# Kernel optimization log

Measured on AMD Instinct MI355X. Metric: run time of the kernel, lower is better.

The kernel has to match this reference:

```python
import jax, jax.numpy as jnp
import numpy as np

D = 512  # token_dim == hidden_dim
K = 65536  # number of trajectory tokens


def safe_normalize(v, eps=1e-6):
    n = jnp.linalg.norm(v, axis=-1, keepdims=True)
    ok = n > eps
    e1 = jnp.zeros_like(v).at[..., 0].set(1.0)
    return jnp.where(ok, v / jnp.maximum(n, eps), e1)


def rot6d_to_matrix(x, eps=1e-6):
    # x: (K, 6) -> R: (K, 3, 3), rows (a1, b2, a3)
    a1 = safe_normalize(x[..., 0:3], eps)
    a2 = x[..., 3:6]
    proj = jnp.sum(a1 * a2, axis=-1, keepdims=True) * a1
    b2 = safe_normalize(a2 - proj, eps)
    a3 = safe_normalize(jnp.cross(a1, b2), eps)
    b2 = safe_normalize(jnp.cross(a3, a1), eps)
    return jnp.stack((a1, b2, a3), axis=-2)


def geodesic_angle(R_pred, R_gt, eps=1e-8):
    # RtR = R_gt^T @ R_pred, per-element (K,3,3)
    RtR = jnp.einsum('kji,kjl->kil', R_gt, R_pred)
    trace = RtR[..., 0, 0] + RtR[..., 1, 1] + RtR[..., 2, 2]
    c = jnp.clip((trace - 1.0) * 0.5, -1.0 + 1e-6, 1.0 - 1e-6)
    skew = RtR - jnp.swapaxes(RtR, -1, -2)
    v = jnp.stack([skew[..., 2, 1], skew[..., 0, 2], skew[..., 1, 0]], axis=-1)
    s = 0.5 * jnp.linalg.norm(v, axis=-1) + eps
    return jnp.arctan2(s, c)


def huber(pred, target, beta, mask):
    # smooth-L1 with beta, masked mean (denominator = clamped mask sum)
    d = jnp.abs(pred - target)
    l = jnp.where(d < beta, 0.5 * d * d / beta, d - 0.5 * beta) * mask
    return l.sum() / jnp.maximum(mask.sum(), 1.0)


def rot_loss_fn(pred, gt):
    # pred, gt: (K, 12) = [L rot6d(6), R rot6d(6)]
    Lp, Rp = pred[:, :6], pred[:, 6:]
    Lt, Rt = gt[:, :6], gt[:, 6:]
    Lvalid = jnp.all(Lt != -1000.0, axis=-1)
    Rvalid = jnp.all(Rt != -1000.0, axis=-1)
    safe6 = jnp.array([1.0, 0.0, 0.0, 0.0, 1.0, 0.0], pred.dtype)
    Lt = jnp.where(Lvalid[:, None], Lt, safe6)
    Rt = jnp.where(Rvalid[:, None], Rt, safe6)
    ang_L = geodesic_angle(rot6d_to_matrix(Lp), rot6d_to_matrix(Lt))
    ang_R = geodesic_angle(rot6d_to_matrix(Rp), rot6d_to_matrix(Rt))
    wL = Lvalid.astype(pred.dtype)
    wR = Rvalid.astype(pred.dtype)
    denom = jnp.maximum(wL.sum() + wR.sum(), 1e-8)
    num = jnp.sum(wL * jnp.where(Lvalid, ang_L, 0.0)) + jnp.sum(wR * jnp.where(Rvalid, ang_R, 0.0))
    return num / denom


def _heads(hidden_states, w1, b1, w2, b2, w3, b3):
    # 4 stacked MLPs (m = time, coord, coord2d, quat), torch Linear layout (out, in)
    h1 = jax.nn.relu(jnp.einsum('kc,mhc->mkh', hidden_states, w1) + b1[:, None, :])
    h2 = jax.nn.relu(jnp.einsum('mkh,mgh->mkg', h1, w2) + b2[:, None, :])
    pred_time = h2[0] @ w3[0:1].T + b3[0:1]      # (K, 1)
    pred_coords = h2[1] @ w3[1:7].T + b3[1:7]    # (K, 6)
    pred_2d = h2[2] @ w3[7:11].T + b3[7:11]      # (K, 4)
    pred_quat = h2[3] @ w3[11:23].T + b3[11:23]  # (K, 12)
    return pred_time, pred_coords, pred_2d, pred_quat


def _loss(pred_time, pred_coords, pred_2d, pred_quat, gt,
          beta_3d=0.07, beta_2d=0.02, beta_time=3.0, sigma_time=3.0):
    time_gt = gt[:, 0:1]
    time_valid = (time_gt != -1000.0).astype(jnp.float32)
    xyz_gt = gt[:, 1:7]
    xyz_valid = (xyz_gt != -1000.0).astype(jnp.float32)
    uv_gt = gt[:, 7:11]
    uv_valid = (uv_gt != -1000.0).astype(jnp.float32)
    quat_gt = gt[:, 11:23]
    quat_valid = (quat_gt != -1000.0).astype(jnp.float32)

    time_loss = huber(pred_time, time_gt, beta_time, time_valid)

    dt = jnp.abs(pred_time - time_gt)
    w_t = jnp.where(time_valid.sum() > 0,
                    jnp.exp(-0.5 * (dt / sigma_time) ** 2) * time_valid,
                    jnp.ones_like(pred_time))  # (K, 1), broadcasts over feature dims

    loss_3d = huber(pred_coords, xyz_gt, beta_3d, xyz_valid * w_t)
    loss_2d = huber(pred_2d / 1408.0, uv_gt / 1408.0, beta_2d, uv_valid * w_t)
    quat_huber = huber(pred_quat, quat_gt, 0.2, quat_valid * w_t)
    rot_l = 0.15 * rot_loss_fn(pred_quat, quat_gt)

    return 1.0 * time_loss + 2.0 * loss_3d + 0.5 * loss_2d + 0.5 * quat_huber + rot_l


def setup_inputs() -> dict:
    key = jax.random.key(0)
    ks = jax.random.split(key, 6)
    s = 1.0 / np.sqrt(D)
    return {
        'hidden_states': jax.random.normal(ks[0], (K, D), jnp.float32),
        'gt_traj': jax.random.uniform(ks[1], (K, 23), jnp.float32),
        'w1': jax.random.normal(ks[2], (4, D, D), jnp.float32) * s,
        'b1': jnp.zeros((4, D), jnp.float32),
        'w2': jax.random.normal(ks[3], (4, D, D), jnp.float32) * s,
        'b2': jnp.zeros((4, D), jnp.float32),
        'w3': jax.random.normal(ks[4], (23, D), jnp.float32) * s,
        'b3': jnp.zeros((23,), jnp.float32),
    }


def reference(hidden_states, gt_traj, w1, b1, w2, b2, w3, b3):
    pred_time, pred_coords, pred_2d, pred_quat = _heads(hidden_states, w1, b1, w2, b2, w3, b3)
    total_loss = _loss(pred_time, pred_coords, pred_2d, pred_quat, gt_traj)
    packed = jnp.concatenate(
        [pred_coords.reshape(-1, 2, 3), pred_quat.reshape(-1, 2, 6)], axis=-1
    ).reshape(-1, 18)
    return pred_time, packed, total_loss
```

## Files before the change

kernel.cpp:

```cpp
#include <hip/hip_runtime.h>
#include <math.h>


#define KROWS 65536
#define DH 512

typedef _Float16 f16;
typedef _Float16 half8 __attribute__((ext_vector_type(8)));
typedef float floatx4 __attribute__((ext_vector_type(4)));

#define WS_WF16   0
#define WS_W3F16  4194304
#define WS_PRED2D 4227072
#define WS_PART   5275648

__global__ __launch_bounds__(256) void convert_weights(
    const float* __restrict__ w1, const float* __restrict__ w2,
    const float* __restrict__ w3, f16* __restrict__ wf16, f16* __restrict__ w3f16)
{
  int t = blockIdx.x * 256 + threadIdx.x;
  if (t < 262144) {
    int ml = t >> 15;
    int mm = ml >> 1, l = ml & 1;
    int r = t & 32767;
    int fb = r >> 6;
    int lane = r & 63;
    int nt = fb >> 4, kq = fb & 15;
    int n = nt * 16 + (lane & 15);
    int k = kq * 32 + (lane >> 4) * 8;
    const float* src = (l ? w2 : w1) + (size_t)mm * 262144 + n * 512 + k;
    floatx4 u0 = *(const floatx4*)(src);
    floatx4 u1 = *(const floatx4*)(src + 4);
    half8 h;
    h[0] = (f16)u0[0]; h[1] = (f16)u0[1]; h[2] = (f16)u0[2]; h[3] = (f16)u0[3];
    h[4] = (f16)u1[0]; h[5] = (f16)u1[1]; h[6] = (f16)u1[2]; h[7] = (f16)u1[3];
    *(half8*)(wf16 + (size_t)ml * 262144 + fb * 512 + lane * 8) = h;
  } else {
    int j = t - 262144;
    if (j < 23 * DH) w3f16[j] = (f16)w3[j];
  }
}

__global__ __launch_bounds__(512, 4)
__attribute__((amdgpu_waves_per_eu(4, 4)))
void fused_kernel(
    const float* __restrict__ hidden,
    const f16* __restrict__ wf16,
    const f16* __restrict__ w3f16,
    const float* __restrict__ b1g,
    const float* __restrict__ b2g,
    const float* __restrict__ b3g,
    float* __restrict__ dout,
    float* __restrict__ pred2d)
{
  __shared__ __align__(16) unsigned char smem[65536];

  const int bid = blockIdx.x;
  const int rr  = bid & 7;
  const int m   = rr >> 1;
  const int row_tile = ((bid >> 3) << 1) | (rr & 1);
  const int r0  = row_tile * 64;
  const int tid = threadIdx.x;
  const int w   = __builtin_amdgcn_readfirstlane(tid >> 6);
  const int lane = tid & 63;
  const int l15 = lane & 15;
  const int lg  = lane >> 4;

  const int arow = l15 * 128;
  const int ao   = (lg * 16) ^ ((l15 & 7) << 4);
  auto aread = [&](int g, int mt) -> half8 {
    return *(const half8*)(smem + (g >> 1) * 8192 + mt * 2048 + arow
                           + (ao ^ ((g & 1) << 6)));
  };
  const f16* bptr = wf16 + (size_t)(m * 2) * 262144 + lane * 8;
  auto bload = [&](int l, int g, int nt) -> half8 {
    return *(const half8*)(bptr + l * 262144 + ((w * 4 + nt) * 16 + g) * 512);
  };

  {
    const int row = tid >> 3;
    const int cg  = tid & 7;
    const int sw  = ((cg * 16) ^ ((row & 7) << 4));
    const float* hr = hidden + (size_t)(r0 + row) * DH + cg * 8;
    unsigned char* dst = smem + row * 128 + sw;
#pragma unroll
    for (int kc = 0; kc < 8; ++kc) {
      floatx4 u0 = *(const floatx4*)(hr + kc * 64);
      floatx4 u1 = *(const floatx4*)(hr + kc * 64 + 4);
      half8 p;
      p[0] = (f16)u0[0]; p[1] = (f16)u0[1]; p[2] = (f16)u0[2]; p[3] = (f16)u0[3];
      p[4] = (f16)u1[0]; p[5] = (f16)u1[1]; p[6] = (f16)u1[2]; p[7] = (f16)u1[3];
      *(half8*)(dst + kc * 8192) = p;
    }
  }

  floatx4 acc[4][4];
  const floatx4 zf = {0.f, 0.f, 0.f, 0.f};
  const half8 hz = {(f16)0, (f16)0, (f16)0, (f16)0, (f16)0, (f16)0, (f16)0, (f16)0};

  __syncthreads();

#pragma unroll
  for (int mt = 0; mt < 4; ++mt)
#pragma unroll
    for (int nt = 0; nt < 4; ++nt) acc[mt][nt] = zf;

  {
    half8 c0 = bload(0, 0, 0), c1 = bload(0, 0, 1),
          c2 = bload(0, 0, 2), c3 = bload(0, 0, 3);
#pragma unroll 1
    for (int g = 0; g < 16; ++g) {
      half8 n0, n1, n2, n3;
      if (g < 15) {
        n0 = bload(0, g + 1, 0); n1 = bload(0, g + 1, 1);
        n2 = bload(0, g + 1, 2); n3 = bload(0, g + 1, 3);
      }
#pragma unroll
      for (int mt = 0; mt < 4; ++mt) {
        half8 a = aread(g, mt);
        acc[mt][0] = __builtin_amdgcn_mfma_f32_16x16x32_f16(a, c0, acc[mt][0], 0, 0, 0);
        acc[mt][1] = __builtin_amdgcn_mfma_f32_16x16x32_f16(a, c1, acc[mt][1], 0, 0, 0);
        acc[mt][2] = __builtin_amdgcn_mfma_f32_16x16x32_f16(a, c2, acc[mt][2], 0, 0, 0);
        acc[mt][3] = __builtin_amdgcn_mfma_f32_16x16x32_f16(a, c3, acc[mt][3], 0, 0, 0);
      }
      c0 = n0; c1 = n1; c2 = n2; c3 = n3;
    }
  }

  __syncthreads();

  {
    unsigned char* myc = smem + w * 8192;
#pragma unroll
    for (int nt = 0; nt < 4; ++nt) {
      const float bv = b1g[m * DH + w * 64 + nt * 16 + l15];
      const int cb = 2 * (nt * 16 + l15);
#pragma unroll
      for (int mt = 0; mt < 4; ++mt)
#pragma unroll
        for (int j = 0; j < 4; ++j) {
          float v = fmaxf(acc[mt][nt][j] + bv, 0.f);
          int row = mt * 16 + 4 * lg + j;
          *(f16*)(myc + row * 128 + (cb ^ ((row & 7) << 4))) = (f16)v;
        }
    }
  }
  __syncthreads();

#pragma unroll
  for (int mt = 0; mt < 4; ++mt)
#pragma unroll
    for (int nt = 0; nt < 4; ++nt) acc[mt][nt] = zf;

  {
    half8 c0 = bload(1, 0, 0), c1 = bload(1, 0, 1),
          c2 = bload(1, 0, 2), c3 = bload(1, 0, 3);
#pragma unroll 1
    for (int g = 0; g < 16; ++g) {
      half8 n0, n1, n2, n3;
      if (g < 15) {
        n0 = bload(1, g + 1, 0); n1 = bload(1, g + 1, 1);
        n2 = bload(1, g + 1, 2); n3 = bload(1, g + 1, 3);
      }
#pragma unroll
      for (int mt = 0; mt < 4; ++mt) {
        half8 a = aread(g, mt);
        acc[mt][0] = __builtin_amdgcn_mfma_f32_16x16x32_f16(a, c0, acc[mt][0], 0, 0, 0);
        acc[mt][1] = __builtin_amdgcn_mfma_f32_16x16x32_f16(a, c1, acc[mt][1], 0, 0, 0);
        acc[mt][2] = __builtin_amdgcn_mfma_f32_16x16x32_f16(a, c2, acc[mt][2], 0, 0, 0);
        acc[mt][3] = __builtin_amdgcn_mfma_f32_16x16x32_f16(a, c3, acc[mt][3], 0, 0, 0);
      }
      c0 = n0; c1 = n1; c2 = n2; c3 = n3;
    }
  }

  __syncthreads();

  {
    unsigned char* myc = smem + w * 8192;
#pragma unroll
    for (int nt = 0; nt < 4; ++nt) {
      const float bv = b2g[m * DH + w * 64 + nt * 16 + l15];
      const int cb = 2 * (nt * 16 + l15);
#pragma unroll
      for (int mt = 0; mt < 4; ++mt)
#pragma unroll
        for (int j = 0; j < 4; ++j) {
          float v = fmaxf(acc[mt][nt][j] + bv, 0.f);
          int row = mt * 16 + 4 * lg + j;
          *(f16*)(myc + row * 128 + (cb ^ ((row & 7) << 4))) = (f16)v;
        }
    }
  }
  __syncthreads();

  if (w < 4) {
    const int base_m = (m == 0) ? 0 : (m == 1) ? 1 : (m == 2) ? 7 : 11;
    const int cnt_m  = (m == 0) ? 1 : (m == 1) ? 6 : (m == 2) ? 4 : 12;
    const bool ovalid = l15 < cnt_m;
    const f16* w3row = w3f16 + (size_t)(base_m + (ovalid ? l15 : 0)) * DH;
    floatx4 acc3 = zf;
#pragma unroll 2
    for (int q = 0; q < 16; ++q) {
      half8 ah = aread(q, w);
      half8 wv = ovalid ? *(const half8*)(w3row + q * 32 + lg * 8) : hz;
      acc3 = __builtin_amdgcn_mfma_f32_16x16x32_f16(ah, wv, acc3, 0, 0, 0);
    }
    if (ovalid) {
      const float bo = b3g[base_m + l15];
#pragma unroll
      for (int j = 0; j < 4; ++j) {
        const int row = r0 + w * 16 + 4 * lg + j;
        const float v = acc3[j] + bo;
        if (m == 0)      { if (l15 == 0) dout[row] = v; }
        else if (m == 1) { dout[KROWS + row * 18 + (l15 < 3 ? l15 : l15 + 6)] = v; }
        else if (m == 2) { pred2d[row * 4 + l15] = v; }
        else             { dout[KROWS + row * 18 + (l15 < 6 ? l15 + 3 : l15 + 6)] = v; }
      }
    }
  }
}

__device__ __forceinline__ void safe_norm3(float x, float y, float z, float* o) {
  float n = sqrtf(x * x + y * y + z * z);
  if (n > 1e-6f) { o[0] = x / n; o[1] = y / n; o[2] = z / n; }
  else           { o[0] = 1.f;   o[1] = 0.f;   o[2] = 0.f; }
}

__device__ __forceinline__ void rot6d(const float* x, float* R) {
  float a1[3]; safe_norm3(x[0], x[1], x[2], a1);
  float d = a1[0] * x[3] + a1[1] * x[4] + a1[2] * x[5];
  float b2[3]; safe_norm3(x[3] - d * a1[0], x[4] - d * a1[1], x[5] - d * a1[2], b2);
  float a3[3];
  safe_norm3(a1[1] * b2[2] - a1[2] * b2[1],
             a1[2] * b2[0] - a1[0] * b2[2],
             a1[0] * b2[1] - a1[1] * b2[0], a3);
  float bb[3];
  safe_norm3(a3[1] * a1[2] - a3[2] * a1[1],
             a3[2] * a1[0] - a3[0] * a1[2],
             a3[0] * a1[1] - a3[1] * a1[0], bb);
  R[0] = a1[0]; R[1] = a1[1]; R[2] = a1[2];
  R[3] = bb[0]; R[4] = bb[1]; R[5] = bb[2];
  R[6] = a3[0]; R[7] = a3[1]; R[8] = a3[2];
}

__device__ __forceinline__ float geo_angle(const float* P, const float* G) {
  float M[9];
#pragma unroll
  for (int i = 0; i < 3; ++i)
#pragma unroll
    for (int l = 0; l < 3; ++l)
      M[i * 3 + l] = G[0 + i] * P[0 + l] + G[3 + i] * P[3 + l] + G[6 + i] * P[6 + l];
  float tr = M[0] + M[4] + M[8];
  float c = fminf(fmaxf((tr - 1.f) * 0.5f, -1.f + 1e-6f), 1.f - 1e-6f);
  float v0 = M[7] - M[5], v1 = M[2] - M[6], v2 = M[3] - M[1];
  float s = 0.5f * sqrtf(v0 * v0 + v1 * v1 + v2 * v2) + 1e-8f;
  return atan2f(s, c);
}

__global__ __launch_bounds__(256) void loss_partial(
    const float* __restrict__ gt, const float* __restrict__ dout,
    const float* __restrict__ pred2d, float* __restrict__ partials)
{
  const int r = blockIdx.x * 256 + threadIdx.x;
  const float* g  = gt + (size_t)r * 23;
  const float* pk = dout + KROWS + (size_t)r * 18;
  float a[17];

  const float pt = dout[r];
  const float tg = g[0];
  const float tv = (tg != -1000.f) ? 1.f : 0.f;
  const float dt = fabsf(pt - tg);
  a[0] = ((dt < 3.f) ? (0.5f * dt * dt / 3.f) : (dt - 1.5f)) * tv;
  a[1] = tv;
  a[2] = tv;
  const float wt = expf(-0.5f * (dt / 3.f) * (dt / 3.f)) * tv;

  float n3T = 0.f, d3T = 0.f, n3F = 0.f, d3F = 0.f;
#pragma unroll
  for (int j = 0; j < 6; ++j) {
    const float p = pk[j < 3 ? j : j + 6];
    const float q = g[1 + j];
    const float val = (q != -1000.f) ? 1.f : 0.f;
    const float d = fabsf(p - q);
    const float l = (d < 0.07f) ? (0.5f * d * d / 0.07f) : (d - 0.035f);
    n3T += l * val * wt; d3T += val * wt; n3F += l * val; d3F += val;
  }
  a[3] = n3T; a[4] = d3T; a[5] = n3F; a[6] = d3F;

  float n2T = 0.f, d2T = 0.f, n2F = 0.f, d2F = 0.f;
#pragma unroll
  for (int j = 0; j < 4; ++j) {
    const float p = pred2d[(size_t)r * 4 + j];
    const float q = g[7 + j];
    const float val = (q != -1000.f) ? 1.f : 0.f;
    const float d = fabsf(p / 1408.f - q / 1408.f);
    const float l = (d < 0.02f) ? (0.5f * d * d / 0.02f) : (d - 0.01f);
    n2T += l * val * wt; d2T += val * wt; n2F += l * val; d2F += val;
  }
  a[7] = n2T; a[8] = d2T; a[9] = n2F; a[10] = d2F;

  float qp[12];
#pragma unroll
  for (int j = 0; j < 12; ++j) qp[j] = pk[j < 6 ? j + 3 : j + 6];
  float nqT = 0.f, dqT = 0.f, nqF = 0.f, dqF = 0.f;
#pragma unroll
  for (int j = 0; j < 12; ++j) {
    const float q = g[11 + j];
    const float val = (q != -1000.f) ? 1.f : 0.f;
    const float d = fabsf(qp[j] - q);
    const float l = (d < 0.2f) ? (0.5f * d * d / 0.2f) : (d - 0.1f);
    nqT += l * val * wt; dqT += val * wt; nqF += l * val; dqF += val;
  }
  a[11] = nqT; a[12] = dqT; a[13] = nqF; a[14] = dqF;

  bool Lv = true, Rv = true;
#pragma unroll
  for (int j = 0; j < 6; ++j) {
    if (g[11 + j] == -1000.f) Lv = false;
    if (g[17 + j] == -1000.f) Rv = false;
  }
  const float safe6[6] = {1.f, 0.f, 0.f, 0.f, 1.f, 0.f};
  float Lt[6], Rt[6];
#pragma unroll
  for (int j = 0; j < 6; ++j) {
    Lt[j] = Lv ? g[11 + j] : safe6[j];
    Rt[j] = Rv ? g[17 + j] : safe6[j];
  }
  float Rp[9], Rg[9];
  rot6d(qp, Rp);     rot6d(Lt, Rg);
  const float angL = geo_angle(Rp, Rg);
  rot6d(qp + 6, Rp); rot6d(Rt, Rg);
  const float angR = geo_angle(Rp, Rg);
  a[15] = (Lv ? angL : 0.f) + (Rv ? angR : 0.f);
  a[16] = (Lv ? 1.f : 0.f) + (Rv ? 1.f : 0.f);

#pragma unroll
  for (int i = 0; i < 17; ++i) {
    float v = a[i];
#pragma unroll
    for (int off = 32; off > 0; off >>= 1) v += __shfl_down(v, off, 64);
    a[i] = v;
  }
  __shared__ float red[4][17];
  if ((threadIdx.x & 63) == 0) {
    const int wv = threadIdx.x >> 6;
#pragma unroll
    for (int i = 0; i < 17; ++i) red[wv][i] = a[i];
  }
  __syncthreads();
  if (threadIdx.x < 17)
    partials[blockIdx.x * 20 + threadIdx.x] =
        red[0][threadIdx.x] + red[1][threadIdx.x] + red[2][threadIdx.x] + red[3][threadIdx.x];
}

__global__ void loss_final(const float* __restrict__ partials, float* __restrict__ dout)
{
  __shared__ float s[17];
  const int i = threadIdx.x;
  if (i < 17) {
    float v = 0.f;
    for (int b = 0; b < 256; ++b) v += partials[b * 20 + i];
    s[i] = v;
  }
  __syncthreads();
  if (i == 0) {
    const bool flag = s[2] > 0.f;
    const float time_loss = s[0] / fmaxf(s[1], 1.f);
    const float l3 = flag ? s[3] / fmaxf(s[4], 1.f) : s[5] / fmaxf(s[6], 1.f);
    const float l2 = flag ? s[7] / fmaxf(s[8], 1.f) : s[9] / fmaxf(s[10], 1.f);
    const float lq = flag ? s[11] / fmaxf(s[12], 1.f) : s[13] / fmaxf(s[14], 1.f);
    const float rot = 0.15f * (s[15] / fmaxf(s[16], 1e-8f));
    dout[19 * KROWS] = time_loss + 2.f * l3 + 0.5f * l2 + 0.5f * lq + rot;
  }
}

extern "C" void kernel_launch(void* const* d_in, const int* in_sizes, int n_in,
                              void* d_out, int out_size, void* d_ws, size_t ws_size,
                              hipStream_t stream) {
  (void)in_sizes; (void)n_in; (void)out_size; (void)ws_size;
  const float* hidden = (const float*)d_in[0];
  const float* gt     = (const float*)d_in[1];
  const float* w1     = (const float*)d_in[2];
  const float* b1     = (const float*)d_in[3];
  const float* w2     = (const float*)d_in[4];
  const float* b2     = (const float*)d_in[5];
  const float* w3     = (const float*)d_in[6];
  const float* b3     = (const float*)d_in[7];
  float* dout = (float*)d_out;

  unsigned char* ws = (unsigned char*)d_ws;
  f16*   wf16     = (f16*)(ws + WS_WF16);
  f16*   w3f16    = (f16*)(ws + WS_W3F16);
  float* pred2d   = (float*)(ws + WS_PRED2D);
  float* partials = (float*)(ws + WS_PART);

  convert_weights<<<1070, 256, 0, stream>>>(w1, w2, w3, wf16, w3f16);
  fused_kernel<<<4096, 512, 0, stream>>>(hidden, wf16, w3f16, b1, b2, b3, dout, pred2d);
  loss_partial<<<256, 256, 0, stream>>>(gt, dout, pred2d, partials);
  loss_final<<<1, 64, 0, stream>>>(partials, dout);
}
```

Baseline: 396.7 us.

## Switch hidden-layer GEMMs to 32x32x16 MFMA with matching weight layout

Replaces the 16x16x32 MFMA tiling of the two hidden-layer GEMMs with 32x32x16 MFMA instructions (2x2 tiles of 32x32 per wave). The pre-converted f16 weight layout and the LDS read pattern are changed to match the new operand fragments, and the epilogue row mapping is updated. The per-iteration B loads are no longer software-prefetched a step ahead but issued at the top of each of 8 K-steps. The intent is fewer MFMA issues and more operand reuse per instruction, at the risk of exposing global-load latency without the prefetch.

```diff
diff --git a/kernel.cpp b/kernel.cpp
--- a/kernel.cpp
+++ b/kernel.cpp
@@ -8,6 +8,7 @@
 typedef _Float16 f16;
 typedef _Float16 half8 __attribute__((ext_vector_type(8)));
 typedef float floatx4 __attribute__((ext_vector_type(4)));
+typedef float floatx16 __attribute__((ext_vector_type(16)));
 
 #define WS_WF16   0
 #define WS_W3F16  4194304
@@ -25,9 +26,9 @@
     int r = t & 32767;
     int fb = r >> 6;
     int lane = r & 63;
-    int nt = fb >> 4, kq = fb & 15;
-    int n = nt * 16 + (lane & 15);
-    int k = kq * 32 + (lane >> 4) * 8;
+    int nt = fb >> 5, ks = fb & 31;
+    int n = nt * 32 + (lane & 31);
+    int k = ks * 16 + (lane >> 5) * 8;
     const float* src = (l ? w2 : w1) + (size_t)mm * 262144 + n * 512 + k;
     floatx4 u0 = *(const floatx4*)(src);
     floatx4 u1 = *(const floatx4*)(src + 4);
@@ -65,16 +66,26 @@
   const int lane = tid & 63;
   const int l15 = lane & 15;
   const int lg  = lane >> 4;
-
-  const int arow = l15 * 128;
-  const int ao   = (lg * 16) ^ ((l15 & 7) << 4);
-  auto aread = [&](int g, int mt) -> half8 {
-    return *(const half8*)(smem + (g >> 1) * 8192 + mt * 2048 + arow
-                           + (ao ^ ((g & 1) << 6)));
+  const int l31 = lane & 31;
+  const int hi  = lane >> 5;
+
+  const int arow32 = l31 * 128;
+  const int hi16   = hi * 16;
+  const int sw31   = (lane & 7) << 4;
+  auto aread32 = [&](int g, int mt, int ks) -> half8 {
+    return *(const half8*)(smem + g * 8192 + mt * 4096 + arow32
+                           + ((ks * 32 + hi16) ^ sw31));
+  };
+  const int arow16 = l15 * 128;
+  const int ao16   = (lg * 16) ^ ((l15 & 7) << 4);
+  auto aread16 = [&](int q, int mt) -> half8 {
+    return *(const half8*)(smem + (q >> 1) * 8192 + mt * 2048 + arow16
+                           + (ao16 ^ ((q & 1) << 6)));
   };
   const f16* bptr = wf16 + (size_t)(m * 2) * 262144 + lane * 8;
-  auto bload = [&](int l, int g, int nt) -> half8 {
-    return *(const half8*)(bptr + l * 262144 + ((w * 4 + nt) * 16 + g) * 512);
+  auto bload = [&](int l, int g, int ks, int nt) -> half8 {
+    return *(const half8*)(bptr + l * 262144
+                           + (((2 * w + nt) * 32) + (g * 4 + ks)) * 512);
   };
 
   {
@@ -94,36 +105,33 @@
     }
   }
 
-  floatx4 acc[4][4];
-  const floatx4 zf = {0.f, 0.f, 0.f, 0.f};
+  floatx16 acc[2][2];
   const half8 hz = {(f16)0, (f16)0, (f16)0, (f16)0, (f16)0, (f16)0, (f16)0, (f16)0};
 
   __syncthreads();
 
 #pragma unroll
-  for (int mt = 0; mt < 4; ++mt)
-#pragma unroll
-    for (int nt = 0; nt < 4; ++nt) acc[mt][nt] = zf;
-
-  {
-    half8 c0 = bload(0, 0, 0), c1 = bload(0, 0, 1),
-          c2 = bload(0, 0, 2), c3 = bload(0, 0, 3);
+  for (int mt = 0; mt < 2; ++mt)
+#pragma unroll
+    for (int nt = 0; nt < 2; ++nt)
+#pragma unroll
+      for (int e = 0; e < 16; ++e) acc[mt][nt][e] = 0.f;
+
 #pragma unroll 1
-    for (int g = 0; g < 16; ++g) {
-      half8 n0, n1, n2, n3;
-      if (g < 15) {
-        n0 = bload(0, g + 1, 0); n1 = bload(0, g + 1, 1);
-        n2 = bload(0, g + 1, 2); n3 = bload(0, g + 1, 3);
+  for (int g = 0; g < 8; ++g) {
+    half8 b[2][4];
+#pragma unroll
+    for (int nt = 0; nt < 2; ++nt)
+#pragma unroll
+      for (int ks = 0; ks < 4; ++ks) b[nt][ks] = bload(0, g, ks, nt);
+#pragma unroll
+    for (int ks = 0; ks < 4; ++ks) {
+#pragma unroll
+      for (int mt = 0; mt < 2; ++mt) {
+        half8 a = aread32(g, mt, ks);
+        acc[mt][0] = __builtin_amdgcn_mfma_f32_32x32x16_f16(a, b[0][ks], acc[mt][0], 0, 0, 0);
+        acc[mt][1] = __builtin_amdgcn_mfma_f32_32x32x16_f16(a, b[1][ks], acc[mt][1], 0, 0, 0);
       }
-#pragma unroll
-      for (int mt = 0; mt < 4; ++mt) {
-        half8 a = aread(g, mt);
-        acc[mt][0] = __builtin_amdgcn_mfma_f32_16x16x32_f16(a, c0, acc[mt][0], 0, 0, 0);
-        acc[mt][1] = __builtin_amdgcn_mfma_f32_16x16x32_f16(a, c1, acc[mt][1], 0, 0, 0);
-        acc[mt][2] = __builtin_amdgcn_mfma_f32_16x16x32_f16(a, c2, acc[mt][2], 0, 0, 0);
-        acc[mt][3] = __builtin_amdgcn_mfma_f32_16x16x32_f16(a, c3, acc[mt][3], 0, 0, 0);
-      }
-      c0 = n0; c1 = n1; c2 = n2; c3 = n3;
     }
   }
 
@@ -132,15 +140,15 @@
   {
     unsigned char* myc = smem + w * 8192;
 #pragma unroll
-    for (int nt = 0; nt < 4; ++nt) {
-      const float bv = b1g[m * DH + w * 64 + nt * 16 + l15];
-      const int cb = 2 * (nt * 16 + l15);
-#pragma unroll
-      for (int mt = 0; mt < 4; ++mt)
-#pragma unroll
-        for (int j = 0; j < 4; ++j) {
-          float v = fmaxf(acc[mt][nt][j] + bv, 0.f);
-          int row = mt * 16 + 4 * lg + j;
+    for (int nt = 0; nt < 2; ++nt) {
+      const float bv = b1g[m * DH + w * 64 + nt * 32 + l31];
+      const int cb = 2 * (nt * 32 + l31);
+#pragma unroll
+      for (int mt = 0; mt < 2; ++mt)
+#pragma unroll
+        for (int e = 0; e < 16; ++e) {
+          float v = fmaxf(acc[mt][nt][e] + bv, 0.f);
+          int row = mt * 32 + (e & 3) + 8 * (e >> 2) + 4 * hi;
           *(f16*)(myc + row * 128 + (cb ^ ((row & 7) << 4))) = (f16)v;
         }
     }
@@ -148,29 +156,27 @@
   __syncthreads();
 
 #pragma unroll
-  for (int mt = 0; mt < 4; ++mt)
-#pragma unroll
-    for (int nt = 0; nt < 4; ++nt) acc[mt][nt] = zf;
-
-  {
-    half8 c0 = bload(1, 0, 0), c1 = bload(1, 0, 1),
-          c2 = bload(1, 0, 2), c3 = bload(1, 0, 3);
+  for (int mt = 0; mt < 2; ++mt)
+#pragma unroll
+    for (int nt = 0; nt < 2; ++nt)
+#pragma unroll
+      for (int e = 0; e < 16; ++e) acc[mt][nt][e] = 0.f;
+
 #pragma unroll 1
-    for (int g = 0; g < 16; ++g) {
-      half8 n0, n1, n2, n3;
-      if (g < 15) {
-        n0 = bload(1, g + 1, 0); n1 = bload(1, g + 1, 1);
-        n2 = bload(1, g + 1, 2); n3 = bload(1, g + 1, 3);
+  for (int g = 0; g < 8; ++g) {
+    half8 b[2][4];
+#pragma unroll
+    for (int nt = 0; nt < 2; ++nt)
+#pragma unroll
+      for (int ks = 0; ks < 4; ++ks) b[nt][ks] = bload(1, g, ks, nt);
+#pragma unroll
+    for (int ks = 0; ks < 4; ++ks) {
+#pragma unroll
+      for (int mt = 0; mt < 2; ++mt) {
+        half8 a = aread32(g, mt, ks);
+        acc[mt][0] = __builtin_amdgcn_mfma_f32_32x32x16_f16(a, b[0][ks], acc[mt][0], 0, 0, 0);
+        acc[mt][1] = __builtin_amdgcn_mfma_f32_32x32x16_f16(a, b[1][ks], acc[mt][1], 0, 0, 0);
       }
-#pragma unroll
-      for (int mt = 0; mt < 4; ++mt) {
-        half8 a = aread(g, mt);
-        acc[mt][0] = __builtin_amdgcn_mfma_f32_16x16x32_f16(a, c0, acc[mt][0], 0, 0, 0);
-        acc[mt][1] = __builtin_amdgcn_mfma_f32_16x16x32_f16(a, c1, acc[mt][1], 0, 0, 0);
-        acc[mt][2] = __builtin_amdgcn_mfma_f32_16x16x32_f16(a, c2, acc[mt][2], 0, 0, 0);
-        acc[mt][3] = __builtin_amdgcn_mfma_f32_16x16x32_f16(a, c3, acc[mt][3], 0, 0, 0);
-      }
-      c0 = n0; c1 = n1; c2 = n2; c3 = n3;
     }
   }
 
@@ -179,15 +185,15 @@
   {
     unsigned char* myc = smem + w * 8192;
 #pragma unroll
-    for (int nt = 0; nt < 4; ++nt) {
-      const float bv = b2g[m * DH + w * 64 + nt * 16 + l15];
-      const int cb = 2 * (nt * 16 + l15);
-#pragma unroll
-      for (int mt = 0; mt < 4; ++mt)
-#pragma unroll
-        for (int j = 0; j < 4; ++j) {
-          float v = fmaxf(acc[mt][nt][j] + bv, 0.f);
-          int row = mt * 16 + 4 * lg + j;
+    for (int nt = 0; nt < 2; ++nt) {
+      const float bv = b2g[m * DH + w * 64 + nt * 32 + l31];
+      const int cb = 2 * (nt * 32 + l31);
+#pragma unroll
+      for (int mt = 0; mt < 2; ++mt)
+#pragma unroll
+        for (int e = 0; e < 16; ++e) {
+          float v = fmaxf(acc[mt][nt][e] + bv, 0.f);
+          int row = mt * 32 + (e & 3) + 8 * (e >> 2) + 4 * hi;
           *(f16*)(myc + row * 128 + (cb ^ ((row & 7) << 4))) = (f16)v;
         }
     }
@@ -199,10 +205,10 @@
     const int cnt_m  = (m == 0) ? 1 : (m == 1) ? 6 : (m == 2) ? 4 : 12;
     const bool ovalid = l15 < cnt_m;
     const f16* w3row = w3f16 + (size_t)(base_m + (ovalid ? l15 : 0)) * DH;
-    floatx4 acc3 = zf;
+    floatx4 acc3 = {0.f, 0.f, 0.f, 0.f};
 #pragma unroll 2
     for (int q = 0; q < 16; ++q) {
-      half8 ah = aread(q, w);
+      half8 ah = aread16(q, w);
       half8 wv = ovalid ? *(const half8*)(w3row + q * 32 + lg * 8) : hz;
       acc3 = __builtin_amdgcn_mfma_f32_16x16x32_f16(ah, wv, acc3, 0, 0, 0);
     }
```

Result: faster. 356.4 us (median of 2 runs) (-10.2%).
